# Kernel tuning notes

Hardware: AMD Instinct MI355X
Metric: run time of the kernel (lower is better)

Reference implementation:

```python
import jax, jax.numpy as jnp
import numpy as np

D_MODEL = 1024
N_EXPERTS = 8
TOP_K = 2
D_FF = 4 * D_MODEL
BATCH, SEQ = 4, 2048


def setup_inputs() -> dict:
    key = jax.random.key(0)
    ks = jax.random.split(key, 7)
    s = 0.02
    return {
        "x": jax.random.normal(ks[0], (BATCH, SEQ, D_MODEL), dtype=jnp.float32),
        "Wg": jax.random.normal(ks[1], (D_MODEL, N_EXPERTS), dtype=jnp.float32) * s,
        "bg": jnp.zeros((N_EXPERTS,), dtype=jnp.float32),
        "W1": jax.random.normal(ks[2], (N_EXPERTS, D_MODEL, D_FF), dtype=jnp.float32) * s,
        "b1": jnp.zeros((N_EXPERTS, D_FF), dtype=jnp.float32),
        "W2": jax.random.normal(ks[3], (N_EXPERTS, D_FF, D_MODEL), dtype=jnp.float32) * s,
        "b2": jnp.zeros((N_EXPERTS, D_MODEL), dtype=jnp.float32),
    }


def reference(x, Wg, bg, W1, b1, W2, b2):
    B, S, D = x.shape
    T = B * S
    xf = x.reshape(T, D)  # [T, d_model]

    # Gating: top-k over softmax probabilities
    gate_logits = xf @ Wg + bg                      # [T, E]
    probs = jax.nn.softmax(gate_logits, axis=-1)
    weights, indices = jax.lax.top_k(probs, TOP_K)  # [T, K] each

    # Dense combine weights c[t, e] = sum_k weights[t,k] * (indices[t,k]==e)
    E = Wg.shape[1]
    c = jnp.zeros((T, E), dtype=x.dtype).at[jnp.arange(T)[:, None], indices].add(weights)

    # All-expert FFN as batched GEMMs (same math as masked per-expert loop)
    h = jnp.einsum('td,edf->etf', xf, W1) + b1[:, None, :]   # [E, T, d_ff]
    a = jax.nn.gelu(h, approximate=False)
    y = jnp.einsum('etf,efd->etd', a, W2) + b2[:, None, :]   # [E, T, d_model]

    out = jnp.einsum('te,etd->td', c, y).reshape(B, S, D)
    return out, gate_logits
```

## Files before the change

### kernel.cpp

```cpp
#include <hip/hip_runtime.h>
#include <hip/hip_bf16.h>
#include <math.h>

#define D_MODEL 1024
#define N_EXP   8
#define D_FF    4096
#define T_TOK   8192
#define NPAIR   (T_TOK * 2)
#define CAP_ROWS (NPAIR + N_EXP * 128)
#define MAX_TILES (CAP_ROWS / 128)

typedef __attribute__((ext_vector_type(4))) float  f32x4;
typedef __attribute__((ext_vector_type(8))) __bf16 bf16x8;
typedef __attribute__((ext_vector_type(4))) __bf16 bf16x4;

#define OFF_W1T   0
#define OFF_W2T   67108864
#define OFF_H     134217728
#define OFF_XR    276824064
#define OFF_META  312475648
#define M_PAIREXP 0
#define M_PAIRW   65536
#define M_ROW2P   131072
#define M_COUNTS  200704
#define M_PADST   200736
#define M_CURSOR  200768
#define M_T2E     201792
#define M_TROW    202336

__device__ __forceinline__ void async_copy16(const void* g, void* s) {
  __builtin_amdgcn_global_load_lds(
      (const __attribute__((address_space(1))) void*)g,
      (__attribute__((address_space(3))) void*)s, 16, 0, 0);
}

__device__ __forceinline__ float gelu_exact(float v) {
  return 0.5f * v * (1.0f + erff(v * 0.70710678118654752440f));
}

__global__ void k_gate(const float* __restrict__ x, const float* __restrict__ Wg,
                       const float* __restrict__ bg, float* __restrict__ logits_out,
                       int* __restrict__ pairExpert, float* __restrict__ pairW) {
  const int t    = blockIdx.x * 4 + (threadIdx.x >> 6);
  const int lane = threadIdx.x & 63;
  const float* xp = x + (size_t)t * D_MODEL;
  float acc[8];
#pragma unroll
  for (int e = 0; e < 8; e++) acc[e] = 0.f;
#pragma unroll
  for (int i = 0; i < 16; i++) {
    int d = i * 64 + lane;
    float xv = xp[d];
    const float4* wr = (const float4*)(Wg + d * 8);
    float4 w0 = wr[0], w1 = wr[1];
    acc[0] += xv * w0.x; acc[1] += xv * w0.y; acc[2] += xv * w0.z; acc[3] += xv * w0.w;
    acc[4] += xv * w1.x; acc[5] += xv * w1.y; acc[6] += xv * w1.z; acc[7] += xv * w1.w;
  }
#pragma unroll
  for (int e = 0; e < 8; e++)
#pragma unroll
    for (int off = 32; off > 0; off >>= 1) acc[e] += __shfl_down(acc[e], off);
  if (lane == 0) {
    float l[8];
#pragma unroll
    for (int e = 0; e < 8; e++) { l[e] = acc[e] + bg[e]; logits_out[t * 8 + e] = l[e]; }
    float m = l[0];
#pragma unroll
    for (int e = 1; e < 8; e++) m = fmaxf(m, l[e]);
    float p[8], s = 0.f;
#pragma unroll
    for (int e = 0; e < 8; e++) { p[e] = expf(l[e] - m); s += p[e]; }
    float inv = 1.0f / s;
    int i1 = 0;
#pragma unroll
    for (int e = 1; e < 8; e++) if (l[e] > l[i1]) i1 = e;
    int i2 = (i1 == 0) ? 1 : 0;
#pragma unroll
    for (int e = 0; e < 8; e++) if (e != i1 && l[e] > l[i2]) i2 = e;
    pairExpert[t * 2 + 0] = i1; pairW[t * 2 + 0] = p[i1] * inv;
    pairExpert[t * 2 + 1] = i2; pairW[t * 2 + 1] = p[i2] * inv;
  }
}

__global__ void k_init(int* __restrict__ row2pair) {
  int i = blockIdx.x * 256 + threadIdx.x;
  if (i < CAP_ROWS) row2pair[i] = -1;
}

__global__ void k_offsets(const int* __restrict__ pairExpert, int* __restrict__ counts,
                          int* __restrict__ padStart, int* __restrict__ cursor,
                          int* __restrict__ t2e, int* __restrict__ trow) {
  __shared__ int hist[8];
  int tid = threadIdx.x;
  if (tid < 8) hist[tid] = 0;
  __syncthreads();
  for (int i = tid; i < NPAIR; i += 256) atomicAdd(&hist[pairExpert[i]], 1);
  __syncthreads();
  if (tid == 0) {
    int run = 0, nt = 0;
    for (int e = 0; e < 8; e++) {
      counts[e] = hist[e]; padStart[e] = run; cursor[e * 32] = 0;
      int tiles = (hist[e] + 127) >> 7;
      for (int i = 0; i < tiles; i++) { t2e[nt] = e; trow[nt] = run + i * 128; nt++; }
      run += tiles * 128;
    }
    for (; nt < MAX_TILES; nt++) t2e[nt] = -1;
  }
}

__global__ void k_place(const int* __restrict__ pairExpert, const int* __restrict__ padStart,
                        int* __restrict__ cursor, int* __restrict__ row2pair) {
  int p = blockIdx.x * 256 + threadIdx.x;
  if (p >= NPAIR) return;
  int e = pairExpert[p];
  int r = atomicAdd(&cursor[e * 32], 1);
  row2pair[padStart[e] + r] = p;
}

__global__ void k_gather(const float* __restrict__ x, const int* __restrict__ row2pair,
                         __bf16* __restrict__ XR) {
  int row = blockIdx.x;
  int pair = row2pair[row];
  int c = threadIdx.x * 4;
  __bf16* dst = XR + (size_t)row * D_MODEL + c;
  if (pair < 0) {
    bf16x4 z = {(__bf16)0.f, (__bf16)0.f, (__bf16)0.f, (__bf16)0.f};
    *(bf16x4*)dst = z;
  } else {
    int t = pair >> 1;
    float4 v = *(const float4*)(x + (size_t)t * D_MODEL + c);
    bf16x4 o = {(__bf16)v.x, (__bf16)v.y, (__bf16)v.z, (__bf16)v.w};
    *(bf16x4*)dst = o;
  }
}

__global__ void k_convT(const float* __restrict__ in, __bf16* __restrict__ out,
                        int R, int C) {
  __shared__ __bf16 tile[64][65];
  int e = blockIdx.z;
  const float* ip = in + (size_t)e * R * C;
  __bf16* op = out + (size_t)e * R * C;
  int r0 = blockIdx.y * 64, c0 = blockIdx.x * 64;
#pragma unroll
  for (int i = 0; i < 16; i++) {
    int lin = threadIdx.x + i * 256;
    int lr = lin >> 6, lc = lin & 63;
    tile[lr][lc] = (__bf16)ip[(size_t)(r0 + lr) * C + c0 + lc];
  }
  __syncthreads();
#pragma unroll
  for (int i = 0; i < 16; i++) {
    int lin = threadIdx.x + i * 256;
    int lc = lin >> 6, lr = lin & 63;
    op[(size_t)(c0 + lc) * R + r0 + lr] = tile[lr][lc];
  }
}

__global__ __launch_bounds__(256) void k_gemm1(
    const __bf16* __restrict__ XR, const __bf16* __restrict__ W1T,
    const float* __restrict__ b1, __bf16* __restrict__ H,
    const int* __restrict__ t2e, const int* __restrict__ trow) {
  __shared__ __align__(16) __bf16 sA[128 * 32];
  __shared__ __align__(16) __bf16 sB[128 * 32];
  const int mt = blockIdx.y;
  const int e = t2e[mt];
  if (e < 0) return;
  const int rowBase = trow[mt];
  const int n0 = blockIdx.x * 128;
  const __bf16* Ab = XR + (size_t)rowBase * D_MODEL;
  const __bf16* Bb = W1T + (size_t)e * D_FF * D_MODEL + (size_t)n0 * D_MODEL;

  const int tid = threadIdx.x;
  const int rA = tid >> 2;
  const int kA = (tid & 3) * 8;
  const int lane = tid & 63;
  const int wave = tid >> 6;
  const int wm = (wave >> 1) * 64, wn = (wave & 1) * 64;
  const int lrow = lane & 15, quad = lane >> 4;

  f32x4 acc[4][4];
#pragma unroll
  for (int i = 0; i < 4; i++)
#pragma unroll
    for (int j = 0; j < 4; j++) acc[i][j] = (f32x4){0.f, 0.f, 0.f, 0.f};

  for (int k0 = 0; k0 < D_MODEL; k0 += 32) {
    async_copy16(Ab + (size_t)rA * D_MODEL + k0 + kA,        (char*)sA + tid * 16);
    async_copy16(Ab + (size_t)(rA + 64) * D_MODEL + k0 + kA, (char*)sA + tid * 16 + 4096);
    async_copy16(Bb + (size_t)rA * D_MODEL + k0 + kA,        (char*)sB + tid * 16);
    async_copy16(Bb + (size_t)(rA + 64) * D_MODEL + k0 + kA, (char*)sB + tid * 16 + 4096);
    __syncthreads();
    bf16x8 af[4], bfr[4];
#pragma unroll
    for (int i = 0; i < 4; i++) af[i]  = *(const bf16x8*)(sA + (wm + i * 16 + lrow) * 32 + quad * 8);
#pragma unroll
    for (int j = 0; j < 4; j++) bfr[j] = *(const bf16x8*)(sB + (wn + j * 16 + lrow) * 32 + quad * 8);
#pragma unroll
    for (int i = 0; i < 4; i++)
#pragma unroll
      for (int j = 0; j < 4; j++)
        acc[i][j] = __builtin_amdgcn_mfma_f32_16x16x32_bf16(af[i], bfr[j], acc[i][j], 0, 0, 0);
    __syncthreads();
  }
#pragma unroll
  for (int j = 0; j < 4; j++) {
    int col = n0 + wn + j * 16 + lrow;
    float bias = b1[e * D_FF + col];
#pragma unroll
    for (int i = 0; i < 4; i++) {
      size_t rowg = (size_t)rowBase + wm + i * 16 + quad * 4;
#pragma unroll
      for (int r = 0; r < 4; r++) {
        float v = acc[i][j][r] + bias;
        H[(rowg + r) * D_FF + col] = (__bf16)gelu_exact(v);
      }
    }
  }
}

__global__ __launch_bounds__(256) void k_gemm2(
    const __bf16* __restrict__ H, const __bf16* __restrict__ W2T,
    const float* __restrict__ b2, float* __restrict__ Ypair,
    const int* __restrict__ row2pair, const float* __restrict__ pairW,
    const int* __restrict__ t2e, const int* __restrict__ trow) {
  __shared__ __align__(16) __bf16 sA[128 * 32];
  __shared__ __align__(16) __bf16 sB[128 * 32];
  const int b = blockIdx.x;
  const int mt = (b >> 6) * 8 + (b & 7);
  const int nb = (b >> 3) & 7;
  const int e = t2e[mt];
  if (e < 0) return;
  const int rowBase = trow[mt];
  const int n0 = nb * 128;
  const __bf16* Ab = H + (size_t)rowBase * D_FF;
  const __bf16* Bb = W2T + (size_t)e * D_MODEL * D_FF + (size_t)n0 * D_FF;

  const int tid = threadIdx.x;
  const int rA = tid >> 2;
  const int kA = (tid & 3) * 8;
  const int lane = tid & 63;
  const int wave = tid >> 6;
  const int wm = (wave >> 1) * 64, wn = (wave & 1) * 64;
  const int lrow = lane & 15, quad = lane >> 4;

  f32x4 acc[4][4];
#pragma unroll
  for (int i = 0; i < 4; i++)
#pragma unroll
    for (int j = 0; j < 4; j++) acc[i][j] = (f32x4){0.f, 0.f, 0.f, 0.f};

  for (int k0 = 0; k0 < D_FF; k0 += 32) {
    async_copy16(Ab + (size_t)rA * D_FF + k0 + kA,        (char*)sA + tid * 16);
    async_copy16(Ab + (size_t)(rA + 64) * D_FF + k0 + kA, (char*)sA + tid * 16 + 4096);
    async_copy16(Bb + (size_t)rA * D_FF + k0 + kA,        (char*)sB + tid * 16);
    async_copy16(Bb + (size_t)(rA + 64) * D_FF + k0 + kA, (char*)sB + tid * 16 + 4096);
    __syncthreads();
    bf16x8 af[4], bfr[4];
#pragma unroll
    for (int i = 0; i < 4; i++) af[i]  = *(const bf16x8*)(sA + (wm + i * 16 + lrow) * 32 + quad * 8);
#pragma unroll
    for (int j = 0; j < 4; j++) bfr[j] = *(const bf16x8*)(sB + (wn + j * 16 + lrow) * 32 + quad * 8);
#pragma unroll
    for (int i = 0; i < 4; i++)
#pragma unroll
      for (int j = 0; j < 4; j++)
        acc[i][j] = __builtin_amdgcn_mfma_f32_16x16x32_bf16(af[i], bfr[j], acc[i][j], 0, 0, 0);
    __syncthreads();
  }
  float bias[4];
#pragma unroll
  for (int j = 0; j < 4; j++) bias[j] = b2[e * D_MODEL + n0 + wn + j * 16 + lrow];
#pragma unroll
  for (int i = 0; i < 4; i++) {
#pragma unroll
    for (int r = 0; r < 4; r++) {
      int rglob = rowBase + wm + i * 16 + quad * 4 + r;
      int pair = row2pair[rglob];
      if (pair < 0) continue;
      float w = pairW[pair];
#pragma unroll
      for (int j = 0; j < 4; j++) {
        int col = n0 + wn + j * 16 + lrow;
        Ypair[(size_t)pair * D_MODEL + col] = w * (acc[i][j][r] + bias[j]);
      }
    }
  }
}

__global__ void k_combine(const float* __restrict__ Ypair, float* __restrict__ out) {
  size_t idx = (size_t)blockIdx.x * 256 + threadIdx.x;
  size_t t = idx >> 8, c4 = idx & 255;
  const float4* y4 = (const float4*)Ypair;
  float4 a = y4[(2 * t) * 256 + c4];
  float4 b = y4[(2 * t + 1) * 256 + c4];
  float4 o = {a.x + b.x, a.y + b.y, a.z + b.z, a.w + b.w};
  ((float4*)out)[idx] = o;
}

extern "C" void kernel_launch(void* const* d_in, const int* in_sizes, int n_in,
                              void* d_out, int out_size, void* d_ws, size_t ws_size,
                              hipStream_t stream) {
  const float* x  = (const float*)d_in[0];
  const float* Wg = (const float*)d_in[1];
  const float* bg = (const float*)d_in[2];
  const float* W1 = (const float*)d_in[3];
  const float* b1 = (const float*)d_in[4];
  const float* W2 = (const float*)d_in[5];
  const float* b2 = (const float*)d_in[6];
  float* out        = (float*)d_out;
  float* logits_out = out + (size_t)T_TOK * D_MODEL;

  char* ws = (char*)d_ws;
  __bf16* W1T = (__bf16*)(ws + OFF_W1T);
  __bf16* W2T = (__bf16*)(ws + OFF_W2T);
  __bf16* H   = (__bf16*)(ws + OFF_H);
  __bf16* XR  = (__bf16*)(ws + OFF_XR);
  float* Ypair = (float*)(ws + OFF_W1T);
  char* meta = ws + OFF_META;
  int*   pairExpert = (int*)(meta + M_PAIREXP);
  float* pairW      = (float*)(meta + M_PAIRW);
  int*   row2pair   = (int*)(meta + M_ROW2P);
  int*   counts     = (int*)(meta + M_COUNTS);
  int*   padStart   = (int*)(meta + M_PADST);
  int*   cursor     = (int*)(meta + M_CURSOR);
  int*   t2e        = (int*)(meta + M_T2E);
  int*   trow       = (int*)(meta + M_TROW);

  k_convT<<<dim3(D_FF / 64, D_MODEL / 64, N_EXP), 256, 0, stream>>>(W1, W1T, D_MODEL, D_FF);
  k_convT<<<dim3(D_MODEL / 64, D_FF / 64, N_EXP), 256, 0, stream>>>(W2, W2T, D_FF, D_MODEL);

  k_init<<<(CAP_ROWS + 255) / 256, 256, 0, stream>>>(row2pair);
  k_gate<<<T_TOK / 4, 256, 0, stream>>>(x, Wg, bg, logits_out, pairExpert, pairW);
  k_offsets<<<1, 256, 0, stream>>>(pairExpert, counts, padStart, cursor, t2e, trow);
  k_place<<<NPAIR / 256, 256, 0, stream>>>(pairExpert, padStart, cursor, row2pair);
  k_gather<<<CAP_ROWS, 256, 0, stream>>>(x, row2pair, XR);

  k_gemm1<<<dim3(D_FF / 128, MAX_TILES), 256, 0, stream>>>(XR, W1T, b1, H, t2e, trow);
  k_gemm2<<<MAX_TILES * (D_MODEL / 128), 256, 0, stream>>>(H, W2T, b2, Ypair, row2pair, pairW, t2e, trow);
  k_combine<<<(size_t)T_TOK * D_MODEL / 4 / 256, 256, 0, stream>>>(Ypair, out);
}
```

Measured before the change: 890.6 us.

## Use 32x32x16 MFMA, tanh-approx GELU, and vectorized weight transpose

Both expert GEMMs move from 16x16x32 MFMA tiles to 32x32x16 MFMA with 2x2 accumulator blocks per wave. This halves the LDS fragment reads and the instruction count per k-step. The exact erf GELU is swapped for a sigmoid form of the tanh approximation using fast exp and rcp, which changes numerics slightly. The weight convert-transpose kernel now uses float4 loads and bf16x4 stores with a padded shared tile, cutting per-element global traffic.

```diff
diff --git a/kernel.cpp b/kernel.cpp
--- a/kernel.cpp
+++ b/kernel.cpp
@@ -10,9 +10,10 @@
 #define CAP_ROWS (NPAIR + N_EXP * 128)
 #define MAX_TILES (CAP_ROWS / 128)
 
-typedef __attribute__((ext_vector_type(4))) float  f32x4;
-typedef __attribute__((ext_vector_type(8))) __bf16 bf16x8;
-typedef __attribute__((ext_vector_type(4))) __bf16 bf16x4;
+typedef __attribute__((ext_vector_type(4)))  float  f32x4;
+typedef __attribute__((ext_vector_type(16))) float  f32x16;
+typedef __attribute__((ext_vector_type(8)))  __bf16 bf16x8;
+typedef __attribute__((ext_vector_type(4)))  __bf16 bf16x4;
 
 #define OFF_W1T   0
 #define OFF_W2T   67108864
@@ -34,8 +35,9 @@
       (__attribute__((address_space(3))) void*)s, 16, 0, 0);
 }
 
-__device__ __forceinline__ float gelu_exact(float v) {
-  return 0.5f * v * (1.0f + erff(v * 0.70710678118654752440f));
+__device__ __forceinline__ float gelu_fast(float v) {
+  float u = 1.5957691216057308f * (v + 0.044715f * v * v * v);
+  return v * __builtin_amdgcn_rcpf(1.f + __expf(-u));
 }
 
 __global__ void k_gate(const float* __restrict__ x, const float* __restrict__ Wg,
@@ -136,23 +138,25 @@
 
 __global__ void k_convT(const float* __restrict__ in, __bf16* __restrict__ out,
                         int R, int C) {
-  __shared__ __bf16 tile[64][65];
+  __shared__ __bf16 tile[64][68];
   int e = blockIdx.z;
-  const float* ip = in + (size_t)e * R * C;
-  __bf16* op = out + (size_t)e * R * C;
-  int r0 = blockIdx.y * 64, c0 = blockIdx.x * 64;
-#pragma unroll
-  for (int i = 0; i < 16; i++) {
-    int lin = threadIdx.x + i * 256;
-    int lr = lin >> 6, lc = lin & 63;
-    tile[lr][lc] = (__bf16)ip[(size_t)(r0 + lr) * C + c0 + lc];
+  const float* ip = in + (size_t)e * R * C + (size_t)(blockIdx.y * 64) * C + blockIdx.x * 64;
+  __bf16* op = out + (size_t)e * R * C + (size_t)(blockIdx.x * 64) * R + blockIdx.y * 64;
+#pragma unroll
+  for (int it = 0; it < 4; it++) {
+    int idx = it * 1024 + threadIdx.x * 4;
+    int lr = idx >> 6, lc = idx & 63;
+    float4 v = *(const float4*)(ip + (size_t)lr * C + lc);
+    bf16x4 o = {(__bf16)v.x, (__bf16)v.y, (__bf16)v.z, (__bf16)v.w};
+    *(bf16x4*)&tile[lr][lc] = o;
   }
   __syncthreads();
 #pragma unroll
-  for (int i = 0; i < 16; i++) {
-    int lin = threadIdx.x + i * 256;
-    int lc = lin >> 6, lr = lin & 63;
-    op[(size_t)(c0 + lc) * R + r0 + lr] = tile[lr][lc];
+  for (int it = 0; it < 4; it++) {
+    int idx = it * 1024 + threadIdx.x * 4;
+    int lc = idx >> 6, lr = idx & 63;
+    bf16x4 o = {tile[lr + 0][lc], tile[lr + 1][lc], tile[lr + 2][lc], tile[lr + 3][lc]};
+    *(bf16x4*)(op + (size_t)lc * R + lr) = o;
   }
 }
 
@@ -176,13 +180,14 @@
   const int lane = tid & 63;
   const int wave = tid >> 6;
   const int wm = (wave >> 1) * 64, wn = (wave & 1) * 64;
-  const int lrow = lane & 15, quad = lane >> 4;
-
-  f32x4 acc[4][4];
-#pragma unroll
-  for (int i = 0; i < 4; i++)
-#pragma unroll
-    for (int j = 0; j < 4; j++) acc[i][j] = (f32x4){0.f, 0.f, 0.f, 0.f};
+  const int l31 = lane & 31;
+  const int half = lane >> 5;
+
+  f32x16 acc[2][2];
+#pragma unroll
+  for (int i = 0; i < 2; i++)
+#pragma unroll
+    for (int j = 0; j < 2; j++) acc[i][j] = (f32x16)(0.f);
 
   for (int k0 = 0; k0 < D_MODEL; k0 += 32) {
     async_copy16(Ab + (size_t)rA * D_MODEL + k0 + kA,        (char*)sA + tid * 16);
@@ -190,32 +195,38 @@
     async_copy16(Bb + (size_t)rA * D_MODEL + k0 + kA,        (char*)sB + tid * 16);
     async_copy16(Bb + (size_t)(rA + 64) * D_MODEL + k0 + kA, (char*)sB + tid * 16 + 4096);
     __syncthreads();
-    bf16x8 af[4], bfr[4];
-#pragma unroll
-    for (int i = 0; i < 4; i++) af[i]  = *(const bf16x8*)(sA + (wm + i * 16 + lrow) * 32 + quad * 8);
-#pragma unroll
-    for (int j = 0; j < 4; j++) bfr[j] = *(const bf16x8*)(sB + (wn + j * 16 + lrow) * 32 + quad * 8);
-#pragma unroll
-    for (int i = 0; i < 4; i++)
-#pragma unroll
-      for (int j = 0; j < 4; j++)
-        acc[i][j] = __builtin_amdgcn_mfma_f32_16x16x32_bf16(af[i], bfr[j], acc[i][j], 0, 0, 0);
+    bf16x8 af[2][2], bfr[2][2];
+#pragma unroll
+    for (int ti = 0; ti < 2; ti++)
+#pragma unroll
+      for (int kc = 0; kc < 2; kc++) {
+        af[ti][kc]  = *(const bf16x8*)(sA + (wm + ti * 32 + l31) * 32 + kc * 16 + half * 8);
+        bfr[ti][kc] = *(const bf16x8*)(sB + (wn + ti * 32 + l31) * 32 + kc * 16 + half * 8);
+      }
+#pragma unroll
+    for (int kc = 0; kc < 2; kc++)
+#pragma unroll
+      for (int ti = 0; ti < 2; ti++)
+#pragma unroll
+        for (int tj = 0; tj < 2; tj++)
+          acc[ti][tj] = __builtin_amdgcn_mfma_f32_32x32x16_bf16(af[ti][kc], bfr[tj][kc], acc[ti][tj], 0, 0, 0);
     __syncthreads();
   }
-#pragma unroll
-  for (int j = 0; j < 4; j++) {
-    int col = n0 + wn + j * 16 + lrow;
-    float bias = b1[e * D_FF + col];
-#pragma unroll
-    for (int i = 0; i < 4; i++) {
-      size_t rowg = (size_t)rowBase + wm + i * 16 + quad * 4;
-#pragma unroll
-      for (int r = 0; r < 4; r++) {
-        float v = acc[i][j][r] + bias;
-        H[(rowg + r) * D_FF + col] = (__bf16)gelu_exact(v);
-      }
+  int   colv[2]; float biasv[2];
+#pragma unroll
+  for (int tj = 0; tj < 2; tj++) {
+    colv[tj] = n0 + wn + tj * 32 + l31;
+    biasv[tj] = b1[e * D_FF + colv[tj]];
+  }
+#pragma unroll
+  for (int ti = 0; ti < 2; ti++)
+#pragma unroll
+    for (int r = 0; r < 16; r++) {
+      size_t row = (size_t)rowBase + wm + ti * 32 + (r & 3) + 8 * (r >> 2) + 4 * half;
+#pragma unroll
+      for (int tj = 0; tj < 2; tj++)
+        H[row * D_FF + colv[tj]] = (__bf16)gelu_fast(acc[ti][tj][r] + biasv[tj]);
     }
-  }
 }
 
 __global__ __launch_bounds__(256) void k_gemm2(
@@ -241,13 +252,14 @@
   const int lane = tid & 63;
   const int wave = tid >> 6;
   const int wm = (wave >> 1) * 64, wn = (wave & 1) * 64;
-  const int lrow = lane & 15, quad = lane >> 4;
-
-  f32x4 acc[4][4];
-#pragma unroll
-  for (int i = 0; i < 4; i++)
-#pragma unroll
-    for (int j = 0; j < 4; j++) acc[i][j] = (f32x4){0.f, 0.f, 0.f, 0.f};
+  const int l31 = lane & 31;
+  const int half = lane >> 5;
+
+  f32x16 acc[2][2];
+#pragma unroll
+  for (int i = 0; i < 2; i++)
+#pragma unroll
+    for (int j = 0; j < 2; j++) acc[i][j] = (f32x16)(0.f);
 
   for (int k0 = 0; k0 < D_FF; k0 += 32) {
     async_copy16(Ab + (size_t)rA * D_FF + k0 + kA,        (char*)sA + tid * 16);
@@ -255,36 +267,41 @@
     async_copy16(Bb + (size_t)rA * D_FF + k0 + kA,        (char*)sB + tid * 16);
     async_copy16(Bb + (size_t)(rA + 64) * D_FF + k0 + kA, (char*)sB + tid * 16 + 4096);
     __syncthreads();
-    bf16x8 af[4], bfr[4];
-#pragma unroll
-    for (int i = 0; i < 4; i++) af[i]  = *(const bf16x8*)(sA + (wm + i * 16 + lrow) * 32 + quad * 8);
-#pragma unroll
-    for (int j = 0; j < 4; j++) bfr[j] = *(const bf16x8*)(sB + (wn + j * 16 + lrow) * 32 + quad * 8);
-#pragma unroll
-    for (int i = 0; i < 4; i++)
-#pragma unroll
-      for (int j = 0; j < 4; j++)
-        acc[i][j] = __builtin_amdgcn_mfma_f32_16x16x32_bf16(af[i], bfr[j], acc[i][j], 0, 0, 0);
+    bf16x8 af[2][2], bfr[2][2];
+#pragma unroll
+    for (int ti = 0; ti < 2; ti++)
+#pragma unroll
+      for (int kc = 0; kc < 2; kc++) {
+        af[ti][kc]  = *(const bf16x8*)(sA + (wm + ti * 32 + l31) * 32 + kc * 16 + half * 8);
+        bfr[ti][kc] = *(const bf16x8*)(sB + (wn + ti * 32 + l31) * 32 + kc * 16 + half * 8);
+      }
+#pragma unroll
+    for (int kc = 0; kc < 2; kc++)
+#pragma unroll
+      for (int ti = 0; ti < 2; ti++)
+#pragma unroll
+        for (int tj = 0; tj < 2; tj++)
+          acc[ti][tj] = __builtin_amdgcn_mfma_f32_32x32x16_bf16(af[ti][kc], bfr[tj][kc], acc[ti][tj], 0, 0, 0);
     __syncthreads();
   }
-  float bias[4];
-#pragma unroll
-  for (int j = 0; j < 4; j++) bias[j] = b2[e * D_MODEL + n0 + wn + j * 16 + lrow];
-#pragma unroll
-  for (int i = 0; i < 4; i++) {
-#pragma unroll
-    for (int r = 0; r < 4; r++) {
-      int rglob = rowBase + wm + i * 16 + quad * 4 + r;
-      int pair = row2pair[rglob];
+  int colv[2]; float biasv[2];
+#pragma unroll
+  for (int tj = 0; tj < 2; tj++) {
+    colv[tj] = n0 + wn + tj * 32 + l31;
+    biasv[tj] = b2[e * D_MODEL + colv[tj]];
+  }
+#pragma unroll
+  for (int ti = 0; ti < 2; ti++)
+#pragma unroll
+    for (int r = 0; r < 16; r++) {
+      int row = rowBase + wm + ti * 32 + (r & 3) + 8 * (r >> 2) + 4 * half;
+      int pair = row2pair[row];
       if (pair < 0) continue;
       float w = pairW[pair];
 #pragma unroll
-      for (int j = 0; j < 4; j++) {
-        int col = n0 + wn + j * 16 + lrow;
-        Ypair[(size_t)pair * D_MODEL + col] = w * (acc[i][j][r] + bias[j]);
-      }
+      for (int tj = 0; tj < 2; tj++)
+        Ypair[(size_t)pair * D_MODEL + colv[tj]] = w * (acc[ti][tj][r] + biasv[tj]);
     }
-  }
 }
 
 __global__ void k_combine(const float* __restrict__ Ypair, float* __restrict__ out) {
```

Result: faster. 864.1 us (-3.0%).
